# Kernel tuning notes

Measured on AMD Instinct MI355X. Metric: run time of the kernel, lower is better.

Reference implementation:

```python
import jax, jax.numpy as jnp
import numpy as np

N_NODES = 100000
N_EDGES = 1600000
NFEAT, NHID, NCLASS = 64, 128, 32


def _glorot(key, shape):
    fan_in, fan_out = shape[0], shape[1]
    lim = np.sqrt(6.0 / (fan_in + fan_out))
    return jax.random.uniform(key, shape, jnp.float32, -lim, lim)


def setup_inputs() -> dict:
    key = jax.random.key(0)
    ks = jax.random.split(key, 12)
    x = jax.random.normal(ks[0], (N_NODES, NFEAT), jnp.float32)
    edge_idx = jax.random.randint(ks[1], (2, N_EDGES), 0, N_NODES, jnp.int64)
    edge_weight = jax.random.uniform(ks[2], (N_EDGES,), jnp.float32)
    return {
        "x": x,
        "edge_idx": edge_idx,
        "edge_weight": edge_weight,
        # SAGEConv 1: out = mean_agg(x) @ Wl1 + b1 + x @ Wr1
        "Wl1": _glorot(ks[3], (NFEAT, NHID)),
        "Wr1": _glorot(ks[4], (NFEAT, NHID)),
        "b1": jnp.zeros((NHID,), jnp.float32),
        # SAGEConv 2
        "Wl2": _glorot(ks[5], (NHID, NHID)),
        "Wr2": _glorot(ks[6], (NHID, NHID)),
        "b2": jnp.zeros((NHID,), jnp.float32),
        # fc head: Linear(nhid, nclass) -> Linear(nclass, 1)
        "Wfc1": _glorot(ks[7], (NHID, NCLASS)),
        "bfc1": jnp.zeros((NCLASS,), jnp.float32),
        "Wfc2": _glorot(ks[8], (NCLASS, 1)),
        "bfc2": jnp.zeros((1,), jnp.float32),
    }


def _sage_conv(x, src, dst, Wl, Wr, b, n_nodes):
    # mean aggregation of source features at destination nodes
    msg_sum = jax.ops.segment_sum(x[src], dst, num_segments=n_nodes)  # [N, d]
    deg = jax.ops.segment_sum(jnp.ones((src.shape[0], 1), x.dtype), dst,
                              num_segments=n_nodes)                    # [N, 1]
    mean = msg_sum / jnp.maximum(deg, 1.0)
    return mean @ Wl + b + x @ Wr


def reference(x, edge_idx, edge_weight, Wl1, Wr1, b1, Wl2, Wr2, b2,
              Wfc1, bfc1, Wfc2, bfc2):
    n_nodes = x.shape[0]
    src, dst = edge_idx[0], edge_idx[1]
    # dropout is identity in eval mode (training=False)
    h = _sage_conv(x, src, dst, Wl1, Wr1, b1, n_nodes)   # [N, nhid]
    h = _sage_conv(h, src, dst, Wl2, Wr2, b2, n_nodes)   # [N, nhid]
    h = h @ Wfc1 + bfc1                                   # [N, nclass]
    out = h @ Wfc2 + bfc2                                 # [N, 1]
    return out
```

## Files before the change

kernel.cpp:

```cpp
#include <hip/hip_runtime.h>

#define S_SHIFT 8
#define S_NODES 256
#define NBKT    400
#define CAP     5120
#define CHUNK   8192
#define NREP    8
#define FTH     512
#define NDOTS   160

__global__ __launch_bounds__(FTH) void fused_kernel(
    const float* __restrict__ x,
    const int* __restrict__ src, const int* __restrict__ dst,
    int E, int N, int B, int nscat,
    int* __restrict__ cursor, unsigned* __restrict__ bucket,
    const float* __restrict__ Wl1, const float* __restrict__ Wr1, const float* __restrict__ b1,
    const float* __restrict__ Wl2, const float* __restrict__ Wr2, const float* __restrict__ b2,
    const float* __restrict__ Wfc1, const float* __restrict__ bfc1,
    const float* __restrict__ Wfc2, const float* __restrict__ bfc2,
    float* __restrict__ ga, float2* __restrict__ gbc, float* __restrict__ c01)
{
    __shared__ int hist[NBKT], lbase[NBKT], lcur[NBKT];
    __shared__ __align__(16) float wv[192];
    __shared__ float uu[128], vl2[128], vr2[128], w2[32];
    int t = threadIdx.x;
    int l = t & 63;
    int w = t >> 6;

    if ((int)blockIdx.x < nscat) {
        int e0 = blockIdx.x * CHUNK;
        int cnt = E - e0; if (cnt > CHUNK) cnt = CHUNK;
        for (int i = t; i < B; i += FTH) hist[i] = 0;
        __syncthreads();
        for (int i = t; i < cnt; i += FTH)
            atomicAdd(&hist[dst[e0 + i] >> S_SHIFT], 1);
        __syncthreads();
        for (int i = t; i < B; i += FTH) {
            lcur[i] = 0;
            if (hist[i] > 0) lbase[i] = atomicAdd(&cursor[i], hist[i]);
        }
        __syncthreads();
        for (int i = t; i < cnt; i += FTH) {
            int d = dst[e0 + i], s = src[e0 + i];
            int bb = d >> S_SHIFT;
            int off = atomicAdd(&lcur[bb], 1);
            bucket[(size_t)bb * CAP + (unsigned)(lbase[bb] + off)] =
                ((unsigned)s << S_SHIFT) | (unsigned)(d & (S_NODES - 1));
        }
    } else {
        if (t < 32) w2[t] = Wfc2[t];
        __syncthreads();
        for (int j = 0; j < 16; ++j) {
            int i = w + 8 * j;
            float p = (l < 32) ? Wfc1[i * 32 + l] * w2[l] : 0.f;
            for (int m = 16; m; m >>= 1) p += __shfl_xor(p, m);
            if (l == 0) uu[i] = p;
        }
        __syncthreads();
        for (int j = 0; j < 16; ++j) {
            int i = w + 8 * j;
            float ua = uu[l], ub = uu[64 + l];
            float pa = Wl2[i * 128 + l] * ua + Wl2[i * 128 + 64 + l] * ub;
            float pb = Wr2[i * 128 + l] * ua + Wr2[i * 128 + 64 + l] * ub;
            for (int m = 32; m; m >>= 1) { pa += __shfl_xor(pa, m); pb += __shfl_xor(pb, m); }
            if (l == 0) { vl2[i] = pa; vr2[i] = pb; }
        }
        __syncthreads();
        for (int j = 0; j < 8; ++j) {
            int i = w + 8 * j;
            float l1a = Wl1[i * 128 + l], l1b = Wl1[i * 128 + 64 + l];
            float r1a = Wr1[i * 128 + l], r1b = Wr1[i * 128 + 64 + l];
            float La = vl2[l], Lb = vl2[64 + l], Ra = vr2[l], Rb = vr2[64 + l];
            float pc = l1a * La + l1b * Lb;
            float pb = l1a * Ra + l1b * Rb + r1a * La + r1b * Lb;
            float pa = r1a * Ra + r1b * Rb;
            for (int m = 32; m; m >>= 1) {
                pa += __shfl_xor(pa, m); pb += __shfl_xor(pb, m); pc += __shfl_xor(pc, m);
            }
            if (l == 0) { wv[i] = pa; wv[64 + i] = pb; wv[128 + i] = pc; }
        }
        if ((int)blockIdx.x == nscat && w == 7) {
            float p0 = b1[l] * vr2[l] + b1[64 + l] * vr2[64 + l]
                     + b2[l] * uu[l] + b2[64 + l] * uu[64 + l];
            if (l < 32) p0 += bfc1[l] * w2[l];
            float p1 = b1[l] * vl2[l] + b1[64 + l] * vl2[64 + l];
            for (int m = 32; m; m >>= 1) { p0 += __shfl_xor(p0, m); p1 += __shfl_xor(p1, m); }
            if (l == 0) { c01[0] = p0 + bfc2[0]; c01[1] = p1; }
        }
        __syncthreads();

        int fp = l & 15, sub = l >> 4;
        float4 wa4 = ((const float4*)wv)[fp];
        float4 wb4 = ((const float4*)wv)[16 + fp];
        float4 wc4 = ((const float4*)wv)[32 + fp];
        const float4* x4 = (const float4*)x;
        int Q = (N + 3) >> 2;
        for (int qd = ((int)blockIdx.x - nscat) * 8 + w; qd < Q; qd += NDOTS * 8) {
            int node = qd * 4 + sub;
            float a = 0.f, b = 0.f, c = 0.f;
            if (node < N) {
                float4 v = x4[(size_t)node * 16 + fp];
                a = v.x * wa4.x + v.y * wa4.y + v.z * wa4.z + v.w * wa4.w;
                b = v.x * wb4.x + v.y * wb4.y + v.z * wb4.z + v.w * wb4.w;
                c = v.x * wc4.x + v.y * wc4.y + v.z * wc4.z + v.w * wc4.w;
            }
            for (int m = 8; m; m >>= 1) {
                a += __shfl_xor(a, m); b += __shfl_xor(b, m); c += __shfl_xor(c, m);
            }
            if (fp == 0 && node < N) { ga[node] = a; gbc[node] = make_float2(b, c); }
        }
    }
}

__global__ __launch_bounds__(512) void aggA_kernel(
    const unsigned* __restrict__ bucket, const int* __restrict__ cursor,
    const float2* __restrict__ gbc,
    float* __restrict__ sB0, float* __restrict__ sC0, int* __restrict__ cnt0,
    float* __restrict__ sB1, float* __restrict__ sC1, int* __restrict__ cnt1, int N)
{
    __shared__ float aB[NREP][S_NODES], aC[NREP][S_NODES];
    __shared__ int cnt[NREP][S_NODES];
    int t = threadIdx.x, blk = blockIdx.x;
    int b = blk >> 1, hi = blk & 1;
    int r = t >> 6;
    float* aBf = (float*)aB; float* aCf = (float*)aC; int* cnf = (int*)cnt;
    for (int i = t; i < NREP * S_NODES; i += 512) { aBf[i] = 0.f; aCf[i] = 0.f; cnf[i] = 0; }
    __syncthreads();
    int n = cursor[b];
    int half = (((n + 1) >> 1) + 3) & ~3;
    if (half > n) half = n;
    int start = hi ? half : 0;
    int end   = hi ? n    : half;
    const unsigned* bp = bucket + (size_t)b * CAP;
    int m = end - start;
    int m4 = m & ~3;
    for (int i = start + 4 * t; i < start + m4; i += 4 * 512) {
        uint4 e4 = *(const uint4*)(bp + i);
        float2 g0 = gbc[e4.x >> S_SHIFT];
        float2 g1 = gbc[e4.y >> S_SHIFT];
        float2 g2 = gbc[e4.z >> S_SHIFT];
        float2 g3 = gbc[e4.w >> S_SHIFT];
        int d0 = e4.x & (S_NODES - 1), d1 = e4.y & (S_NODES - 1);
        int d2 = e4.z & (S_NODES - 1), d3 = e4.w & (S_NODES - 1);
        atomicAdd(&aB[r][d0], g0.x); atomicAdd(&aC[r][d0], g0.y); atomicAdd(&cnt[r][d0], 1);
        atomicAdd(&aB[r][d1], g1.x); atomicAdd(&aC[r][d1], g1.y); atomicAdd(&cnt[r][d1], 1);
        atomicAdd(&aB[r][d2], g2.x); atomicAdd(&aC[r][d2], g2.y); atomicAdd(&cnt[r][d2], 1);
        atomicAdd(&aB[r][d3], g3.x); atomicAdd(&aC[r][d3], g3.y); atomicAdd(&cnt[r][d3], 1);
    }
    int it = start + m4 + t;
    if (it < end) {
        unsigned uu = bp[it];
        float2 g = gbc[uu >> S_SHIFT];
        int dl = uu & (S_NODES - 1);
        atomicAdd(&aB[r][dl], g.x); atomicAdd(&aC[r][dl], g.y); atomicAdd(&cnt[r][dl], 1);
    }
    __syncthreads();
    if (t < S_NODES) {
        int node = (b << S_SHIFT) + t;
        if (node < N) {
            float sb = 0.f, sc = 0.f; int d = 0;
            #pragma unroll
            for (int k = 0; k < NREP; ++k) { sb += aB[k][t]; sc += aC[k][t]; d += cnt[k][t]; }
            if (hi == 0) { sB0[node] = sb; sC0[node] = sc; cnt0[node] = d; }
            else         { sB1[node] = sb; sC1[node] = sc; cnt1[node] = d; }
        }
    }
}

__global__ __launch_bounds__(512) void finalize_kernel(
    const float* __restrict__ sB0, const float* __restrict__ sC0, const int* __restrict__ cnt0,
    const float* __restrict__ sB1, const float* __restrict__ sC1, const int* __restrict__ cnt1,
    const float* __restrict__ ga, const float* __restrict__ c01,
    float* __restrict__ q, float* __restrict__ inv, float* __restrict__ out, int N)
{
    int node = blockIdx.x * 512 + threadIdx.x;
    if (node < N) {
        int d = cnt0[node] + cnt1[node];
        float sb = sB0[node] + sB1[node];
        float sc = sC0[node] + sC1[node];
        float iv = 1.0f / ((d > 0) ? (float)d : 1.0f);
        q[node]   = iv * sc;
        inv[node] = iv;
        out[node] = ga[node] + iv * sb + c01[0] + (d > 0 ? c01[1] : 0.f);
    }
}

__global__ __launch_bounds__(512) void aggB_kernel(
    const unsigned* __restrict__ bucket, const int* __restrict__ cursor,
    const float* __restrict__ q, const float* __restrict__ inv,
    float* __restrict__ out, int N)
{
    __shared__ float a2[NREP][S_NODES];
    int t = threadIdx.x, blk = blockIdx.x;
    int b = blk >> 1, hi = blk & 1;
    int r = t >> 6;
    float* a2f = (float*)a2;
    for (int i = t; i < NREP * S_NODES; i += 512) a2f[i] = 0.f;
    __syncthreads();
    int n = cursor[b];
    int half = (((n + 1) >> 1) + 3) & ~3;
    if (half > n) half = n;
    int start = hi ? half : 0;
    int end   = hi ? n    : half;
    const unsigned* bp = bucket + (size_t)b * CAP;
    int m = end - start;
    int m4 = m & ~3;
    for (int i = start + 4 * t; i < start + m4; i += 4 * 512) {
        uint4 e4 = *(const uint4*)(bp + i);
        float q0 = q[e4.x >> S_SHIFT], q1 = q[e4.y >> S_SHIFT];
        float q2 = q[e4.z >> S_SHIFT], q3 = q[e4.w >> S_SHIFT];
        atomicAdd(&a2[r][e4.x & (S_NODES - 1)], q0);
        atomicAdd(&a2[r][e4.y & (S_NODES - 1)], q1);
        atomicAdd(&a2[r][e4.z & (S_NODES - 1)], q2);
        atomicAdd(&a2[r][e4.w & (S_NODES - 1)], q3);
    }
    int it = start + m4 + t;
    if (it < end) {
        unsigned uu = bp[it];
        atomicAdd(&a2[r][uu & (S_NODES - 1)], q[uu >> S_SHIFT]);
    }
    __syncthreads();
    if (t < S_NODES) {
        int node = (b << S_SHIFT) + t;
        if (node < N) {
            float s2 = 0.f;
            #pragma unroll
            for (int k = 0; k < NREP; ++k) s2 += a2[k][t];
            atomicAdd(&out[node], inv[node] * s2);
        }
    }
}

extern "C" void kernel_launch(void* const* d_in, const int* in_sizes, int n_in,
                              void* d_out, int out_size, void* d_ws, size_t ws_size,
                              hipStream_t stream) {
    const float* x    = (const float*)d_in[0];
    const int*   eidx = (const int*)d_in[1];
    const float* Wl1  = (const float*)d_in[3];
    const float* Wr1  = (const float*)d_in[4];
    const float* b1   = (const float*)d_in[5];
    const float* Wl2  = (const float*)d_in[6];
    const float* Wr2  = (const float*)d_in[7];
    const float* b2   = (const float*)d_in[8];
    const float* Wfc1 = (const float*)d_in[9];
    const float* bfc1 = (const float*)d_in[10];
    const float* Wfc2 = (const float*)d_in[11];
    const float* bfc2 = (const float*)d_in[12];

    const int N = in_sizes[0] / 64;
    const int E = in_sizes[2];
    const int* src = eidx;
    const int* dst = eidx + E;
    const int B = (N + S_NODES - 1) >> S_SHIFT;
    const int nscat = (E + CHUNK - 1) / CHUNK;

    char* ws = (char*)d_ws;
    size_t o = 0;
    auto take = [&](size_t bytes) { char* p = ws + o; o += (bytes + 127) & ~(size_t)127; return p; };
    int*      cursor = (int*)take(NBKT * 4);
    float*    c01    = (float*)take(64);
    float*    ga     = (float*)take((size_t)N * 4);
    float*    q      = (float*)take((size_t)N * 4);
    float*    inv    = (float*)take((size_t)N * 4);
    float*    sB0    = (float*)take((size_t)N * 4);
    float*    sC0    = (float*)take((size_t)N * 4);
    int*      cnt0   = (int*)take((size_t)N * 4);
    float*    sB1    = (float*)take((size_t)N * 4);
    float*    sC1    = (float*)take((size_t)N * 4);
    int*      cnt1   = (int*)take((size_t)N * 4);
    float2*   gbc    = (float2*)take((size_t)N * 8);
    unsigned* bucket = (unsigned*)take((size_t)B * CAP * 4);

    hipMemsetAsync(cursor, 0, NBKT * 4, stream);

    fused_kernel<<<nscat + NDOTS, FTH, 0, stream>>>(
        x, src, dst, E, N, B, nscat, cursor, bucket,
        Wl1, Wr1, b1, Wl2, Wr2, b2, Wfc1, bfc1, Wfc2, bfc2,
        ga, gbc, c01);

    aggA_kernel<<<2 * B, 512, 0, stream>>>(bucket, cursor, gbc,
                                           sB0, sC0, cnt0, sB1, sC1, cnt1, N);

    finalize_kernel<<<(N + 511) / 512, 512, 0, stream>>>(
        sB0, sC0, cnt0, sB1, sC1, cnt1, ga, c01, q, inv, (float*)d_out, N);

    aggB_kernel<<<2 * B, 512, 0, stream>>>(bucket, cursor, q, inv, (float*)d_out, N);
}
```

Measured before the change: 172.5 us.

## Merge four kernels into one cooperative persistent kernel with grid syncs

Replaces the four separate launches (scatter/dot, aggregate A, finalize, aggregate B) with a single cooperative persistent kernel that loops over tasks and separates the phases with grid.sync, using a union of shared-memory layouts. It also halves the scatter chunk size and raises the dot-task count so work spreads over the persistent grid. The aim is to remove launch overhead and inter-kernel gaps. In exchange it adds grid-wide barrier cost, possibly lower occupancy from the union shared-memory footprint, and a hardcoded CU count (NCU 256) used to size the cooperative grid.

```diff
diff --git a/kernel.cpp b/kernel.cpp
--- a/kernel.cpp
+++ b/kernel.cpp
@@ -1,15 +1,27 @@
 #include <hip/hip_runtime.h>
+#include <hip/hip_cooperative_groups.h>
+
+namespace cg = cooperative_groups;
 
 #define S_SHIFT 8
 #define S_NODES 256
 #define NBKT    400
 #define CAP     5120
-#define CHUNK   8192
+#define CHUNK   4096
 #define NREP    8
-#define FTH     512
-#define NDOTS   160
-
-__global__ __launch_bounds__(FTH) void fused_kernel(
+#define TPB     512
+#define NDOT    633
+#define MAXGRID 1024
+#define NCU     256
+
+union __align__(16) SMem {
+    struct { int hist[NBKT], lbase[NBKT], lcur[NBKT]; } sc;
+    struct { float wv[192], uu[128], vl2[128], vr2[128], w2[32]; } fo;
+    struct { float aB[NREP][S_NODES], aC[NREP][S_NODES]; int cnt[NREP][S_NODES]; } a1;
+    struct { float a2[NREP][S_NODES]; } ab;
+};
+
+__global__ __launch_bounds__(TPB, 8) void mega_kernel(
     const float* __restrict__ x,
     const int* __restrict__ src, const int* __restrict__ dst,
     int E, int N, int B, int nscat,
@@ -18,215 +30,225 @@
     const float* __restrict__ Wl2, const float* __restrict__ Wr2, const float* __restrict__ b2,
     const float* __restrict__ Wfc1, const float* __restrict__ bfc1,
     const float* __restrict__ Wfc2, const float* __restrict__ bfc2,
-    float* __restrict__ ga, float2* __restrict__ gbc, float* __restrict__ c01)
+    float* __restrict__ ga, float2* __restrict__ gbc, float* __restrict__ c01,
+    float* __restrict__ q, float* __restrict__ inv,
+    float* __restrict__ sB0, float* __restrict__ sC0, int* __restrict__ cnt0,
+    float* __restrict__ sB1, float* __restrict__ sC1, int* __restrict__ cnt1,
+    float* __restrict__ outp)
 {
-    __shared__ int hist[NBKT], lbase[NBKT], lcur[NBKT];
-    __shared__ __align__(16) float wv[192];
-    __shared__ float uu[128], vl2[128], vr2[128], w2[32];
+    __shared__ SMem sm;
+    cg::grid_group grid = cg::this_grid();
     int t = threadIdx.x;
     int l = t & 63;
     int w = t >> 6;
-
-    if ((int)blockIdx.x < nscat) {
-        int e0 = blockIdx.x * CHUNK;
-        int cnt = E - e0; if (cnt > CHUNK) cnt = CHUNK;
-        for (int i = t; i < B; i += FTH) hist[i] = 0;
-        __syncthreads();
-        for (int i = t; i < cnt; i += FTH)
-            atomicAdd(&hist[dst[e0 + i] >> S_SHIFT], 1);
-        __syncthreads();
-        for (int i = t; i < B; i += FTH) {
-            lcur[i] = 0;
-            if (hist[i] > 0) lbase[i] = atomicAdd(&cursor[i], hist[i]);
-        }
-        __syncthreads();
-        for (int i = t; i < cnt; i += FTH) {
-            int d = dst[e0 + i], s = src[e0 + i];
-            int bb = d >> S_SHIFT;
-            int off = atomicAdd(&lcur[bb], 1);
-            bucket[(size_t)bb * CAP + (unsigned)(lbase[bb] + off)] =
-                ((unsigned)s << S_SHIFT) | (unsigned)(d & (S_NODES - 1));
-        }
-    } else {
-        if (t < 32) w2[t] = Wfc2[t];
-        __syncthreads();
-        for (int j = 0; j < 16; ++j) {
-            int i = w + 8 * j;
-            float p = (l < 32) ? Wfc1[i * 32 + l] * w2[l] : 0.f;
-            for (int m = 16; m; m >>= 1) p += __shfl_xor(p, m);
-            if (l == 0) uu[i] = p;
-        }
-        __syncthreads();
-        for (int j = 0; j < 16; ++j) {
-            int i = w + 8 * j;
-            float ua = uu[l], ub = uu[64 + l];
-            float pa = Wl2[i * 128 + l] * ua + Wl2[i * 128 + 64 + l] * ub;
-            float pb = Wr2[i * 128 + l] * ua + Wr2[i * 128 + 64 + l] * ub;
-            for (int m = 32; m; m >>= 1) { pa += __shfl_xor(pa, m); pb += __shfl_xor(pb, m); }
-            if (l == 0) { vl2[i] = pa; vr2[i] = pb; }
-        }
-        __syncthreads();
-        for (int j = 0; j < 8; ++j) {
-            int i = w + 8 * j;
-            float l1a = Wl1[i * 128 + l], l1b = Wl1[i * 128 + 64 + l];
-            float r1a = Wr1[i * 128 + l], r1b = Wr1[i * 128 + 64 + l];
-            float La = vl2[l], Lb = vl2[64 + l], Ra = vr2[l], Rb = vr2[64 + l];
-            float pc = l1a * La + l1b * Lb;
-            float pb = l1a * Ra + l1b * Rb + r1a * La + r1b * Lb;
-            float pa = r1a * Ra + r1b * Rb;
-            for (int m = 32; m; m >>= 1) {
-                pa += __shfl_xor(pa, m); pb += __shfl_xor(pb, m); pc += __shfl_xor(pc, m);
-            }
-            if (l == 0) { wv[i] = pa; wv[64 + i] = pb; wv[128 + i] = pc; }
-        }
-        if ((int)blockIdx.x == nscat && w == 7) {
-            float p0 = b1[l] * vr2[l] + b1[64 + l] * vr2[64 + l]
-                     + b2[l] * uu[l] + b2[64 + l] * uu[64 + l];
-            if (l < 32) p0 += bfc1[l] * w2[l];
-            float p1 = b1[l] * vl2[l] + b1[64 + l] * vl2[64 + l];
-            for (int m = 32; m; m >>= 1) { p0 += __shfl_xor(p0, m); p1 += __shfl_xor(p1, m); }
-            if (l == 0) { c01[0] = p0 + bfc2[0]; c01[1] = p1; }
-        }
-        __syncthreads();
-
-        int fp = l & 15, sub = l >> 4;
-        float4 wa4 = ((const float4*)wv)[fp];
-        float4 wb4 = ((const float4*)wv)[16 + fp];
-        float4 wc4 = ((const float4*)wv)[32 + fp];
-        const float4* x4 = (const float4*)x;
-        int Q = (N + 3) >> 2;
-        for (int qd = ((int)blockIdx.x - nscat) * 8 + w; qd < Q; qd += NDOTS * 8) {
-            int node = qd * 4 + sub;
-            float a = 0.f, b = 0.f, c = 0.f;
-            if (node < N) {
-                float4 v = x4[(size_t)node * 16 + fp];
-                a = v.x * wa4.x + v.y * wa4.y + v.z * wa4.z + v.w * wa4.w;
-                b = v.x * wb4.x + v.y * wb4.y + v.z * wb4.z + v.w * wb4.w;
-                c = v.x * wc4.x + v.y * wc4.y + v.z * wc4.z + v.w * wc4.w;
-            }
-            for (int m = 8; m; m >>= 1) {
-                a += __shfl_xor(a, m); b += __shfl_xor(b, m); c += __shfl_xor(c, m);
-            }
-            if (fp == 0 && node < N) { ga[node] = a; gbc[node] = make_float2(b, c); }
+    int gsz = gridDim.x;
+
+    {
+        int ntask0 = nscat + NDOT;
+        bool folded = false;
+        for (int task = blockIdx.x; task < ntask0; task += gsz) {
+            if (task < nscat) {
+                int e0 = task * CHUNK;
+                int cnt = E - e0; if (cnt > CHUNK) cnt = CHUNK;
+                for (int i = t; i < B; i += TPB) sm.sc.hist[i] = 0;
+                __syncthreads();
+                for (int i = t; i < cnt; i += TPB)
+                    atomicAdd(&sm.sc.hist[dst[e0 + i] >> S_SHIFT], 1);
+                __syncthreads();
+                for (int i = t; i < B; i += TPB) {
+                    sm.sc.lcur[i] = 0;
+                    if (sm.sc.hist[i] > 0) sm.sc.lbase[i] = atomicAdd(&cursor[i], sm.sc.hist[i]);
+                }
+                __syncthreads();
+                for (int i = t; i < cnt; i += TPB) {
+                    int d = dst[e0 + i], s = src[e0 + i];
+                    int bb = d >> S_SHIFT;
+                    int off = atomicAdd(&sm.sc.lcur[bb], 1);
+                    bucket[(size_t)bb * CAP + (unsigned)(sm.sc.lbase[bb] + off)] =
+                        ((unsigned)s << S_SHIFT) | (unsigned)(d & (S_NODES - 1));
+                }
+                __syncthreads();
+            } else {
+                if (!folded) {
+                    folded = true;
+                    if (t < 32) sm.fo.w2[t] = Wfc2[t];
+                    __syncthreads();
+                    for (int j = 0; j < 16; ++j) {
+                        int i = w + 8 * j;
+                        float p = (l < 32) ? Wfc1[i * 32 + l] * sm.fo.w2[l] : 0.f;
+                        for (int m = 16; m; m >>= 1) p += __shfl_xor(p, m);
+                        if (l == 0) sm.fo.uu[i] = p;
+                    }
+                    __syncthreads();
+                    for (int j = 0; j < 16; ++j) {
+                        int i = w + 8 * j;
+                        float ua = sm.fo.uu[l], ub = sm.fo.uu[64 + l];
+                        float pa = Wl2[i * 128 + l] * ua + Wl2[i * 128 + 64 + l] * ub;
+                        float pb = Wr2[i * 128 + l] * ua + Wr2[i * 128 + 64 + l] * ub;
+                        for (int m = 32; m; m >>= 1) { pa += __shfl_xor(pa, m); pb += __shfl_xor(pb, m); }
+                        if (l == 0) { sm.fo.vl2[i] = pa; sm.fo.vr2[i] = pb; }
+                    }
+                    __syncthreads();
+                    for (int j = 0; j < 8; ++j) {
+                        int i = w + 8 * j;
+                        float l1a = Wl1[i * 128 + l], l1b = Wl1[i * 128 + 64 + l];
+                        float r1a = Wr1[i * 128 + l], r1b = Wr1[i * 128 + 64 + l];
+                        float La = sm.fo.vl2[l], Lb = sm.fo.vl2[64 + l];
+                        float Ra = sm.fo.vr2[l], Rb = sm.fo.vr2[64 + l];
+                        float pc = l1a * La + l1b * Lb;
+                        float pb = l1a * Ra + l1b * Rb + r1a * La + r1b * Lb;
+                        float pa = r1a * Ra + r1b * Rb;
+                        for (int m = 32; m; m >>= 1) {
+                            pa += __shfl_xor(pa, m); pb += __shfl_xor(pb, m); pc += __shfl_xor(pc, m);
+                        }
+                        if (l == 0) { sm.fo.wv[i] = pa; sm.fo.wv[64 + i] = pb; sm.fo.wv[128 + i] = pc; }
+                    }
+                    __syncthreads();
+                }
+                if (task == nscat && w == 7) {
+                    float p0 = b1[l] * sm.fo.vr2[l] + b1[64 + l] * sm.fo.vr2[64 + l]
+                             + b2[l] * sm.fo.uu[l] + b2[64 + l] * sm.fo.uu[64 + l];
+                    if (l < 32) p0 += bfc1[l] * sm.fo.w2[l];
+                    float p1 = b1[l] * sm.fo.vl2[l] + b1[64 + l] * sm.fo.vl2[64 + l];
+                    for (int m = 32; m; m >>= 1) { p0 += __shfl_xor(p0, m); p1 += __shfl_xor(p1, m); }
+                    if (l == 0) { c01[0] = p0 + bfc2[0]; c01[1] = p1; }
+                }
+                int dtask = task - nscat;
+                int fp = l & 15, sub = l >> 4;
+                float4 wa4 = ((const float4*)sm.fo.wv)[fp];
+                float4 wb4 = ((const float4*)sm.fo.wv)[16 + fp];
+                float4 wc4 = ((const float4*)sm.fo.wv)[32 + fp];
+                const float4* x4 = (const float4*)x;
+                int Q = (N + 3) >> 2;
+                for (int qd = dtask * 8 + w; qd < Q; qd += NDOT * 8) {
+                    int node = qd * 4 + sub;
+                    float a = 0.f, b = 0.f, c = 0.f;
+                    if (node < N) {
+                        float4 v = x4[(size_t)node * 16 + fp];
+                        a = v.x * wa4.x + v.y * wa4.y + v.z * wa4.z + v.w * wa4.w;
+                        b = v.x * wb4.x + v.y * wb4.y + v.z * wb4.z + v.w * wb4.w;
+                        c = v.x * wc4.x + v.y * wc4.y + v.z * wc4.z + v.w * wc4.w;
+                    }
+                    for (int m = 8; m; m >>= 1) {
+                        a += __shfl_xor(a, m); b += __shfl_xor(b, m); c += __shfl_xor(c, m);
+                    }
+                    if (fp == 0 && node < N) { ga[node] = a; gbc[node] = make_float2(b, c); }
+                }
+            }
         }
     }
-}
-
-__global__ __launch_bounds__(512) void aggA_kernel(
-    const unsigned* __restrict__ bucket, const int* __restrict__ cursor,
-    const float2* __restrict__ gbc,
-    float* __restrict__ sB0, float* __restrict__ sC0, int* __restrict__ cnt0,
-    float* __restrict__ sB1, float* __restrict__ sC1, int* __restrict__ cnt1, int N)
-{
-    __shared__ float aB[NREP][S_NODES], aC[NREP][S_NODES];
-    __shared__ int cnt[NREP][S_NODES];
-    int t = threadIdx.x, blk = blockIdx.x;
-    int b = blk >> 1, hi = blk & 1;
-    int r = t >> 6;
-    float* aBf = (float*)aB; float* aCf = (float*)aC; int* cnf = (int*)cnt;
-    for (int i = t; i < NREP * S_NODES; i += 512) { aBf[i] = 0.f; aCf[i] = 0.f; cnf[i] = 0; }
-    __syncthreads();
-    int n = cursor[b];
-    int half = (((n + 1) >> 1) + 3) & ~3;
-    if (half > n) half = n;
-    int start = hi ? half : 0;
-    int end   = hi ? n    : half;
-    const unsigned* bp = bucket + (size_t)b * CAP;
-    int m = end - start;
-    int m4 = m & ~3;
-    for (int i = start + 4 * t; i < start + m4; i += 4 * 512) {
-        uint4 e4 = *(const uint4*)(bp + i);
-        float2 g0 = gbc[e4.x >> S_SHIFT];
-        float2 g1 = gbc[e4.y >> S_SHIFT];
-        float2 g2 = gbc[e4.z >> S_SHIFT];
-        float2 g3 = gbc[e4.w >> S_SHIFT];
-        int d0 = e4.x & (S_NODES - 1), d1 = e4.y & (S_NODES - 1);
-        int d2 = e4.z & (S_NODES - 1), d3 = e4.w & (S_NODES - 1);
-        atomicAdd(&aB[r][d0], g0.x); atomicAdd(&aC[r][d0], g0.y); atomicAdd(&cnt[r][d0], 1);
-        atomicAdd(&aB[r][d1], g1.x); atomicAdd(&aC[r][d1], g1.y); atomicAdd(&cnt[r][d1], 1);
-        atomicAdd(&aB[r][d2], g2.x); atomicAdd(&aC[r][d2], g2.y); atomicAdd(&cnt[r][d2], 1);
-        atomicAdd(&aB[r][d3], g3.x); atomicAdd(&aC[r][d3], g3.y); atomicAdd(&cnt[r][d3], 1);
-    }
-    int it = start + m4 + t;
-    if (it < end) {
-        unsigned uu = bp[it];
-        float2 g = gbc[uu >> S_SHIFT];
-        int dl = uu & (S_NODES - 1);
-        atomicAdd(&aB[r][dl], g.x); atomicAdd(&aC[r][dl], g.y); atomicAdd(&cnt[r][dl], 1);
-    }
-    __syncthreads();
-    if (t < S_NODES) {
-        int node = (b << S_SHIFT) + t;
-        if (node < N) {
-            float sb = 0.f, sc = 0.f; int d = 0;
-            #pragma unroll
-            for (int k = 0; k < NREP; ++k) { sb += aB[k][t]; sc += aC[k][t]; d += cnt[k][t]; }
-            if (hi == 0) { sB0[node] = sb; sC0[node] = sc; cnt0[node] = d; }
-            else         { sB1[node] = sb; sC1[node] = sc; cnt1[node] = d; }
+    __threadfence();
+    grid.sync();
+
+    {
+        int ntA = 2 * B;
+        for (int tid = blockIdx.x; tid < ntA; tid += gsz) {
+            int b = tid >> 1, hi = tid & 1;
+            int r = t >> 6;
+            float* aBf = (float*)sm.a1.aB; float* aCf = (float*)sm.a1.aC; int* cnf = (int*)sm.a1.cnt;
+            for (int i = t; i < NREP * S_NODES; i += TPB) { aBf[i] = 0.f; aCf[i] = 0.f; cnf[i] = 0; }
+            __syncthreads();
+            int n = cursor[b];
+            int half = (((n + 1) >> 1) + 3) & ~3;
+            if (half > n) half = n;
+            int start = hi ? half : 0;
+            int end   = hi ? n    : half;
+            const unsigned* bp = bucket + (size_t)b * CAP;
+            int m = end - start;
+            int m4 = m & ~3;
+            for (int i = start + 4 * t; i < start + m4; i += 4 * TPB) {
+                uint4 e4 = *(const uint4*)(bp + i);
+                float2 g0 = gbc[e4.x >> S_SHIFT];
+                float2 g1 = gbc[e4.y >> S_SHIFT];
+                float2 g2 = gbc[e4.z >> S_SHIFT];
+                float2 g3 = gbc[e4.w >> S_SHIFT];
+                int d0 = e4.x & (S_NODES - 1), d1 = e4.y & (S_NODES - 1);
+                int d2 = e4.z & (S_NODES - 1), d3 = e4.w & (S_NODES - 1);
+                atomicAdd(&sm.a1.aB[r][d0], g0.x); atomicAdd(&sm.a1.aC[r][d0], g0.y); atomicAdd(&sm.a1.cnt[r][d0], 1);
+                atomicAdd(&sm.a1.aB[r][d1], g1.x); atomicAdd(&sm.a1.aC[r][d1], g1.y); atomicAdd(&sm.a1.cnt[r][d1], 1);
+                atomicAdd(&sm.a1.aB[r][d2], g2.x); atomicAdd(&sm.a1.aC[r][d2], g2.y); atomicAdd(&sm.a1.cnt[r][d2], 1);
+                atomicAdd(&sm.a1.aB[r][d3], g3.x); atomicAdd(&sm.a1.aC[r][d3], g3.y); atomicAdd(&sm.a1.cnt[r][d3], 1);
+            }
+            int it = start + m4 + t;
+            if (it < end) {
+                unsigned uu = bp[it];
+                float2 g = gbc[uu >> S_SHIFT];
+                int dl = uu & (S_NODES - 1);
+                atomicAdd(&sm.a1.aB[r][dl], g.x); atomicAdd(&sm.a1.aC[r][dl], g.y); atomicAdd(&sm.a1.cnt[r][dl], 1);
+            }
+            __syncthreads();
+            if (t < S_NODES) {
+                int node = (b << S_SHIFT) + t;
+                if (node < N) {
+                    float sb = 0.f, sc = 0.f; int d = 0;
+                    #pragma unroll
+                    for (int k = 0; k < NREP; ++k) { sb += sm.a1.aB[k][t]; sc += sm.a1.aC[k][t]; d += sm.a1.cnt[k][t]; }
+                    if (hi == 0) { sB0[node] = sb; sC0[node] = sc; cnt0[node] = d; }
+                    else         { sB1[node] = sb; sC1[node] = sc; cnt1[node] = d; }
+                }
+            }
+            __syncthreads();
         }
     }
-}
-
-__global__ __launch_bounds__(512) void finalize_kernel(
-    const float* __restrict__ sB0, const float* __restrict__ sC0, const int* __restrict__ cnt0,
-    const float* __restrict__ sB1, const float* __restrict__ sC1, const int* __restrict__ cnt1,
-    const float* __restrict__ ga, const float* __restrict__ c01,
-    float* __restrict__ q, float* __restrict__ inv, float* __restrict__ out, int N)
-{
-    int node = blockIdx.x * 512 + threadIdx.x;
-    if (node < N) {
-        int d = cnt0[node] + cnt1[node];
-        float sb = sB0[node] + sB1[node];
-        float sc = sC0[node] + sC1[node];
-        float iv = 1.0f / ((d > 0) ? (float)d : 1.0f);
-        q[node]   = iv * sc;
-        inv[node] = iv;
-        out[node] = ga[node] + iv * sb + c01[0] + (d > 0 ? c01[1] : 0.f);
+    __threadfence();
+    grid.sync();
+
+    {
+        float c0 = c01[0], c1 = c01[1];
+        for (int node = blockIdx.x * TPB + t; node < N; node += gsz * TPB) {
+            int d = cnt0[node] + cnt1[node];
+            float sb = sB0[node] + sB1[node];
+            float sc = sC0[node] + sC1[node];
+            float iv = 1.0f / ((d > 0) ? (float)d : 1.0f);
+            q[node]    = iv * sc;
+            inv[node]  = iv;
+            outp[node] = ga[node] + iv * sb + c0 + (d > 0 ? c1 : 0.f);
+        }
     }
-}
-
-__global__ __launch_bounds__(512) void aggB_kernel(
-    const unsigned* __restrict__ bucket, const int* __restrict__ cursor,
-    const float* __restrict__ q, const float* __restrict__ inv,
-    float* __restrict__ out, int N)
-{
-    __shared__ float a2[NREP][S_NODES];
-    int t = threadIdx.x, blk = blockIdx.x;
-    int b = blk >> 1, hi = blk & 1;
-    int r = t >> 6;
-    float* a2f = (float*)a2;
-    for (int i = t; i < NREP * S_NODES; i += 512) a2f[i] = 0.f;
-    __syncthreads();
-    int n = cursor[b];
-    int half = (((n + 1) >> 1) + 3) & ~3;
-    if (half > n) half = n;
-    int start = hi ? half : 0;
-    int end   = hi ? n    : half;
-    const unsigned* bp = bucket + (size_t)b * CAP;
-    int m = end - start;
-    int m4 = m & ~3;
-    for (int i = start + 4 * t; i < start + m4; i += 4 * 512) {
-        uint4 e4 = *(const uint4*)(bp + i);
-        float q0 = q[e4.x >> S_SHIFT], q1 = q[e4.y >> S_SHIFT];
-        float q2 = q[e4.z >> S_SHIFT], q3 = q[e4.w >> S_SHIFT];
-        atomicAdd(&a2[r][e4.x & (S_NODES - 1)], q0);
-        atomicAdd(&a2[r][e4.y & (S_NODES - 1)], q1);
-        atomicAdd(&a2[r][e4.z & (S_NODES - 1)], q2);
-        atomicAdd(&a2[r][e4.w & (S_NODES - 1)], q3);
-    }
-    int it = start + m4 + t;
-    if (it < end) {
-        unsigned uu = bp[it];
-        atomicAdd(&a2[r][uu & (S_NODES - 1)], q[uu >> S_SHIFT]);
-    }
-    __syncthreads();
-    if (t < S_NODES) {
-        int node = (b << S_SHIFT) + t;
-        if (node < N) {
-            float s2 = 0.f;
-            #pragma unroll
-            for (int k = 0; k < NREP; ++k) s2 += a2[k][t];
-            atomicAdd(&out[node], inv[node] * s2);
+    __threadfence();
+    grid.sync();
+
+    {
+        int ntA = 2 * B;
+        for (int tid = blockIdx.x; tid < ntA; tid += gsz) {
+            int b = tid >> 1, hi = tid & 1;
+            int r = t >> 6;
+            float* a2f = (float*)sm.ab.a2;
+            for (int i = t; i < NREP * S_NODES; i += TPB) a2f[i] = 0.f;
+            __syncthreads();
+            int n = cursor[b];
+            int half = (((n + 1) >> 1) + 3) & ~3;
+            if (half > n) half = n;
+            int start = hi ? half : 0;
+            int end   = hi ? n    : half;
+            const unsigned* bp = bucket + (size_t)b * CAP;
+            int m = end - start;
+            int m4 = m & ~3;
+            for (int i = start + 4 * t; i < start + m4; i += 4 * TPB) {
+                uint4 e4 = *(const uint4*)(bp + i);
+                float q0 = q[e4.x >> S_SHIFT], q1 = q[e4.y >> S_SHIFT];
+                float q2 = q[e4.z >> S_SHIFT], q3 = q[e4.w >> S_SHIFT];
+                atomicAdd(&sm.ab.a2[r][e4.x & (S_NODES - 1)], q0);
+                atomicAdd(&sm.ab.a2[r][e4.y & (S_NODES - 1)], q1);
+                atomicAdd(&sm.ab.a2[r][e4.z & (S_NODES - 1)], q2);
+                atomicAdd(&sm.ab.a2[r][e4.w & (S_NODES - 1)], q3);
+            }
+            int it = start + m4 + t;
+            if (it < end) {
+                unsigned uu = bp[it];
+                atomicAdd(&sm.ab.a2[r][uu & (S_NODES - 1)], q[uu >> S_SHIFT]);
+            }
+            __syncthreads();
+            if (t < S_NODES) {
+                int node = (b << S_SHIFT) + t;
+                if (node < N) {
+                    float s2 = 0.f;
+                    #pragma unroll
+                    for (int k = 0; k < NREP; ++k) s2 += sm.ab.a2[k][t];
+                    atomicAdd(&outp[node], inv[node] * s2);
+                }
+            }
+            __syncthreads();
         }
     }
 }
@@ -273,16 +295,21 @@
 
     hipMemsetAsync(cursor, 0, NBKT * 4, stream);
 
-    fused_kernel<<<nscat + NDOTS, FTH, 0, stream>>>(
-        x, src, dst, E, N, B, nscat, cursor, bucket,
-        Wl1, Wr1, b1, Wl2, Wr2, b2, Wfc1, bfc1, Wfc2, bfc2,
-        ga, gbc, c01);
-
-    aggA_kernel<<<2 * B, 512, 0, stream>>>(bucket, cursor, gbc,
-                                           sB0, sC0, cnt0, sB1, sC1, cnt1, N);
-
-    finalize_kernel<<<(N + 511) / 512, 512, 0, stream>>>(
-        sB0, sC0, cnt0, sB1, sC1, cnt1, ga, c01, q, inv, (float*)d_out, N);
-
-    aggB_kernel<<<2 * B, 512, 0, stream>>>(bucket, cursor, q, inv, (float*)d_out, N);
+    int maxb = 0;
+    if (hipOccupancyMaxActiveBlocksPerMultiprocessor(&maxb, mega_kernel, TPB, 0) != hipSuccess || maxb < 1)
+        maxb = 1;
+    int gridn = maxb * NCU; if (gridn > MAXGRID) gridn = MAXGRID;
+
+    int E_ = E, N_ = N, B_ = B, nscat_ = nscat;
+    void* args[] = {
+        (void*)&x, (void*)&src, (void*)&dst, (void*)&E_, (void*)&N_, (void*)&B_, (void*)&nscat_,
+        (void*)&cursor, (void*)&bucket,
+        (void*)&Wl1, (void*)&Wr1, (void*)&b1, (void*)&Wl2, (void*)&Wr2, (void*)&b2,
+        (void*)&Wfc1, (void*)&bfc1, (void*)&Wfc2, (void*)&bfc2,
+        (void*)&ga, (void*)&gbc, (void*)&c01, (void*)&q, (void*)&inv,
+        (void*)&sB0, (void*)&sC0, (void*)&cnt0, (void*)&sB1, (void*)&sC1, (void*)&cnt1,
+        (void*)&d_out
+    };
+    hipLaunchCooperativeKernel(reinterpret_cast<void*>(mega_kernel),
+                               dim3(gridn), dim3(TPB), args, 0, stream);
 }
```

Measured after the change: 679.1 us. 294% more time.
